# Performance work log

Measured on AMD Instinct MI355X. Metric: run time of the kernel, lower is better.

The kernel has to match this reference:

```python
import jax, jax.numpy as jnp
import numpy as np

C = 512      # channels
COND = 256   # cond_dim
H = 8        # n_heads
D = C // H   # head_dim
EPS = 1e-5


def setup_inputs() -> dict:
    key = jax.random.key(0)
    ks = jax.random.split(key, 16)
    s = 0.02
    inp = {
        "x": jax.random.normal(ks[0], (8, C, 1024), jnp.float32),
        "cond": jax.random.normal(ks[1], (8, COND), jnp.float32),
        "ln_g": jnp.ones((C,), jnp.float32),
        "ln_b": jnp.zeros((C,), jnp.float32),
        "Wq": jax.random.normal(ks[2], (C, C), jnp.float32) * s,
        "bq": jnp.zeros((C,), jnp.float32),
        "Wk": jax.random.normal(ks[3], (C, COND), jnp.float32) * s,
        "bk": jnp.zeros((C,), jnp.float32),
        "Wv": jax.random.normal(ks[4], (C, COND), jnp.float32) * s,
        "bv": jnp.zeros((C,), jnp.float32),
        "in_proj_w": jax.random.normal(ks[5], (3 * C, C), jnp.float32) * s,
        "in_proj_b": jnp.zeros((3 * C,), jnp.float32),
        "out_w": jax.random.normal(ks[6], (C, C), jnp.float32) * s,
        "out_b": jnp.zeros((C,), jnp.float32),
        "proj_w": jax.random.normal(ks[7], (C, C), jnp.float32) * s,
        "proj_b": jnp.zeros((C,), jnp.float32),
    }
    return inp


def _forward(x, cond, ln_g, ln_b, Wq, bq, Wk, bk, Wv, bv,
             in_proj_w, in_proj_b, out_w, out_b, proj_w, proj_b):
    B, _, T = x.shape
    x_seq = jnp.transpose(x, (0, 2, 1))                      # [B,T,C]
    mu = jnp.mean(x_seq, axis=-1, keepdims=True)
    var = jnp.mean((x_seq - mu) ** 2, axis=-1, keepdims=True)
    x_norm = (x_seq - mu) / jnp.sqrt(var + EPS) * ln_g + ln_b

    q = x_norm @ Wq.T + bq                                   # [B,T,C]
    k = cond @ Wk.T + bk                                     # [B,C]
    v = cond @ Wv.T + bv                                     # [B,C]

    # nn.MultiheadAttention internal input projections
    wq2, wk2, wv2 = in_proj_w[:C], in_proj_w[C:2 * C], in_proj_w[2 * C:]
    bq2, bk2, bv2 = in_proj_b[:C], in_proj_b[C:2 * C], in_proj_b[2 * C:]
    q2 = q @ wq2.T + bq2                                     # [B,T,C]
    k2 = k @ wk2.T + bk2                                     # [B,C]
    v2 = v @ wv2.T + bv2                                     # [B,C]

    qh = q2.reshape(B, T, H, D)                              # [B,T,H,D]
    kh = k2.reshape(B, H, D)
    vh = v2.reshape(B, H, D)

    # k/v are expanded to length T in the original module -> [B,T,C]
    k_exp = jnp.broadcast_to(kh[:, None, :, :], (B, T, H, D))
    v_exp = jnp.broadcast_to(vh[:, None, :, :], (B, T, H, D))

    scale = 1.0 / jnp.sqrt(jnp.float32(D))
    scores = jnp.einsum('bthd,bshd->bhts', qh * scale, k_exp)  # [B,H,T,T]
    attn = jax.nn.softmax(scores, axis=-1)
    outh = jnp.einsum('bhts,bshd->bthd', attn, v_exp)          # [B,T,H,D]
    out = outh.reshape(B, T, C) @ out_w.T + out_b              # MHA out_proj

    out = out @ proj_w.T + proj_b                              # self.proj
    out = jnp.transpose(out, (0, 2, 1))                        # [B,C,T]
    return x + out


def reference(x, cond, ln_g, ln_b, Wq, bq, Wk, bk, Wv, bv,
              in_proj_w, in_proj_b, out_w, out_b, proj_w, proj_b):
    return _forward(x, cond, ln_g, ln_b, Wq, bq, Wk, bk, Wv, bv,
                    in_proj_w, in_proj_b, out_w, out_b, proj_w, proj_b)
```

## Files before the change

### kernel.cpp

```cpp
#include <hip/hip_runtime.h>

#define CC   512
#define CONDK 256
#define BB   8
#define TT   1024

template<int K>
__global__ void gemv_kernel(const float* __restrict__ W, const float* __restrict__ bias,
                            const float* __restrict__ in, float* __restrict__ out) {
    const int wave = threadIdx.x >> 6;
    const int lane = threadIdx.x & 63;
    const int c = blockIdx.x * 4 + wave;
    const int b = blockIdx.y;
    const float* wrow = W + (size_t)c * K;
    const float* inb  = in + (size_t)b * K;
    float acc = 0.f;
#pragma unroll
    for (int j = lane; j < K; j += 64)
        acc += wrow[j] * inb[j];
#pragma unroll
    for (int off = 32; off >= 1; off >>= 1)
        acc += __shfl_down(acc, off, 64);
    if (lane == 0)
        out[b * CC + c] = acc + bias[c];
}

__global__ void add_bcast_kernel(const float* __restrict__ x, const float* __restrict__ w,
                                 float* __restrict__ out) {
    const int total4 = BB * CC * TT / 4;
    const float4* x4 = (const float4*)x;
    float4* o4 = (float4*)out;
    for (int i = blockIdx.x * blockDim.x + threadIdx.x; i < total4;
         i += gridDim.x * blockDim.x) {
        const int bc = i >> 8;
        const float a = w[bc];
        float4 v = x4[i];
        v.x += a; v.y += a; v.z += a; v.w += a;
        o4[i] = v;
    }
}

extern "C" void kernel_launch(void* const* d_in, const int* in_sizes, int n_in,
                              void* d_out, int out_size, void* d_ws, size_t ws_size,
                              hipStream_t stream) {
    const float* x         = (const float*)d_in[0];
    const float* cond      = (const float*)d_in[1];
    const float* Wv        = (const float*)d_in[8];
    const float* bv        = (const float*)d_in[9];
    const float* in_proj_w = (const float*)d_in[10];
    const float* in_proj_b = (const float*)d_in[11];
    const float* out_w     = (const float*)d_in[12];
    const float* out_b     = (const float*)d_in[13];
    const float* proj_w    = (const float*)d_in[14];
    const float* proj_b    = (const float*)d_in[15];
    float* out = (float*)d_out;

    float* v1 = (float*)d_ws;
    float* v2 = v1 + BB * CC;
    float* u  = v2 + BB * CC;
    float* w  = u  + BB * CC;

    dim3 blk(256);
    dim3 g1(CC / 4, BB);
    gemv_kernel<CONDK><<<g1, blk, 0, stream>>>(Wv, bv, cond, v1);
    gemv_kernel<CC><<<g1, blk, 0, stream>>>(in_proj_w + 2 * CC * CC, in_proj_b + 2 * CC, v1, v2);
    gemv_kernel<CC><<<g1, blk, 0, stream>>>(out_w, out_b, v2, u);
    gemv_kernel<CC><<<g1, blk, 0, stream>>>(proj_w, proj_b, u, w);

    add_bcast_kernel<<<1024, 256, 0, stream>>>(x, w, out);
}
```

Measured before the change: 22.48 us.

## Precombine proj and out weights, fuse final GEMV with broadcast add

Computes L1 = proj_w·out_w as a 512x512 matrix product and t = proj_w·out_b + proj_b in the first kernel, alongside the cond→v1 GEMV, so the two trailing GEMVs become one. The last GEMV is fused into the broadcast-add kernel, with each wave computing one (b,c) scalar and then streaming its row of x. This cuts five launches to three and removes a dependent GEMV stage. The cost is a full 512^3 weight product recomputed on every call and a different floating-point summation order.

New measurement: 31.14 us. 38.5% more time.

```diff
diff --git a/kernel.cpp b/kernel.cpp
--- a/kernel.cpp
+++ b/kernel.cpp
@@ -1,42 +1,108 @@
 #include <hip/hip_runtime.h>
 
-#define CC   512
-#define CONDK 256
-#define BB   8
-#define TT   1024
+#define CC 512
+#define CK 256
+#define BB 8
+#define TT 1024
 
-template<int K>
-__global__ void gemv_kernel(const float* __restrict__ W, const float* __restrict__ bias,
-                            const float* __restrict__ in, float* __restrict__ out) {
-    const int wave = threadIdx.x >> 6;
-    const int lane = threadIdx.x & 63;
-    const int c = blockIdx.x * 4 + wave;
-    const int b = blockIdx.y;
-    const float* wrow = W + (size_t)c * K;
-    const float* inb  = in + (size_t)b * K;
+__device__ __forceinline__ float wave_allreduce(float v) {
+#pragma unroll
+    for (int m = 1; m < 64; m <<= 1)
+        v += __shfl_xor(v, m, 64);
+    return v;
+}
+
+__global__ void k1_kernel(const float* __restrict__ P, const float* __restrict__ O,
+                          const float* __restrict__ Wv, const float* __restrict__ bv,
+                          const float* __restrict__ ob, const float* __restrict__ pb,
+                          const float* __restrict__ cond,
+                          float* __restrict__ L1, float* __restrict__ t,
+                          float* __restrict__ v1) {
+    const int blk = blockIdx.x;
+    const int tid = threadIdx.x;
+    const int wave = tid >> 6, lane = tid & 63;
+
+    if (blk < 256) {
+        __shared__ float As[32][33];
+        __shared__ float Bs[32][33];
+        const int ti = (blk >> 4) * 32, tj = (blk & 15) * 32;
+        const int lrow = tid >> 3, lc4 = (tid & 7) * 4;
+        const int ty = tid >> 4, tx = tid & 15;
+        float a00 = 0.f, a01 = 0.f, a10 = 0.f, a11 = 0.f;
+        for (int k = 0; k < 512; k += 32) {
+            __syncthreads();
+            *(float4*)&As[lrow][lc4] = *(const float4*)&P[(ti + lrow) * 512 + k + lc4];
+            *(float4*)&Bs[lrow][lc4] = *(const float4*)&O[(k + lrow) * 512 + tj + lc4];
+            __syncthreads();
+#pragma unroll
+            for (int kk = 0; kk < 32; ++kk) {
+                const float x0 = As[2 * ty][kk], x1 = As[2 * ty + 1][kk];
+                const float y0 = Bs[kk][2 * tx], y1 = Bs[kk][2 * tx + 1];
+                a00 += x0 * y0; a01 += x0 * y1; a10 += x1 * y0; a11 += x1 * y1;
+            }
+        }
+        float* d = L1 + (ti + 2 * ty) * 512 + tj + 2 * tx;
+        d[0] = a00; d[1] = a01; d[512] = a10; d[513] = a11;
+    } else if (blk < 384) {
+        const int gw = (blk - 256) * 4 + wave;
+#pragma unroll
+        for (int r = 0; r < 8; ++r) {
+            const int o = gw * 8 + r;
+            const int b = o >> 9, c = o & 511;
+            float acc = 0.f;
+#pragma unroll
+            for (int j = 0; j < CK; j += 64)
+                acc += Wv[c * CK + j + lane] * cond[b * CK + j + lane];
+            acc = wave_allreduce(acc);
+            if (lane == 0) v1[o] = acc + bv[c];
+        }
+    } else {
+        const int c = (blk - 384) * 4 + wave;
+        float acc = 0.f;
+#pragma unroll
+        for (int k = 0; k < CC; k += 64)
+            acc += P[c * CC + k + lane] * ob[k + lane];
+        acc = wave_allreduce(acc);
+        if (lane == 0) t[c] = acc + pb[c];
+    }
+}
+
+__global__ void k2_kernel(const float* __restrict__ wv2, const float* __restrict__ b2,
+                          const float* __restrict__ v1, float* __restrict__ v2) {
+    const int wave = threadIdx.x >> 6, lane = threadIdx.x & 63;
+    const int gw = blockIdx.x * 4 + wave;
+#pragma unroll
+    for (int r = 0; r < 4; ++r) {
+        const int o = gw * 4 + r;
+        const int b = o >> 9, c = o & 511;
+        float acc = 0.f;
+#pragma unroll
+        for (int j = 0; j < CC; j += 64)
+            acc += wv2[c * CC + j + lane] * v1[b * CC + j + lane];
+        acc = wave_allreduce(acc);
+        if (lane == 0) v2[o] = acc + b2[c];
+    }
+}
+
+__global__ void k3_kernel(const float* __restrict__ L1, const float* __restrict__ t,
+                          const float* __restrict__ v2, const float* __restrict__ x,
+                          float* __restrict__ out) {
+    const int wave = threadIdx.x >> 6, lane = threadIdx.x & 63;
+    const int o = blockIdx.x * 4 + wave;
+    const int b = o >> 9, c = o & 511;
     float acc = 0.f;
 #pragma unroll
-    for (int j = lane; j < K; j += 64)
-        acc += wrow[j] * inb[j];
+    for (int j = 0; j < CC; j += 64)
+        acc += L1[c * CC + j + lane] * v2[b * CC + j + lane];
+    const float w = wave_allreduce(acc) + t[c];
+
+    const float4* x4 = (const float4*)x + (size_t)o * (TT / 4);
+    float4* o4 = (float4*)out + (size_t)o * (TT / 4);
 #pragma unroll
-    for (int off = 32; off >= 1; off >>= 1)
-        acc += __shfl_down(acc, off, 64);
-    if (lane == 0)
-        out[b * CC + c] = acc + bias[c];
-}
-
-__global__ void add_bcast_kernel(const float* __restrict__ x, const float* __restrict__ w,
-                                 float* __restrict__ out) {
-    const int total4 = BB * CC * TT / 4;
-    const float4* x4 = (const float4*)x;
-    float4* o4 = (float4*)out;
-    for (int i = blockIdx.x * blockDim.x + threadIdx.x; i < total4;
-         i += gridDim.x * blockDim.x) {
-        const int bc = i >> 8;
-        const float a = w[bc];
-        float4 v = x4[i];
-        v.x += a; v.y += a; v.z += a; v.w += a;
-        o4[i] = v;
+    for (int i = 0; i < TT / 4; i += 64) {
+        float4 v = x4[i + lane];
+        v.x += w; v.y += w; v.z += w; v.w += w;
+        o4[i + lane] = v;
     }
 }
 
@@ -55,17 +121,14 @@
     const float* proj_b    = (const float*)d_in[15];
     float* out = (float*)d_out;
 
-    float* v1 = (float*)d_ws;
+    float* L1 = (float*)d_ws;
+    float* t  = L1 + CC * CC;
+    float* v1 = t + CC;
     float* v2 = v1 + BB * CC;
-    float* u  = v2 + BB * CC;
-    float* w  = u  + BB * CC;
 
-    dim3 blk(256);
-    dim3 g1(CC / 4, BB);
-    gemv_kernel<CONDK><<<g1, blk, 0, stream>>>(Wv, bv, cond, v1);
-    gemv_kernel<CC><<<g1, blk, 0, stream>>>(in_proj_w + 2 * CC * CC, in_proj_b + 2 * CC, v1, v2);
-    gemv_kernel<CC><<<g1, blk, 0, stream>>>(out_w, out_b, v2, u);
-    gemv_kernel<CC><<<g1, blk, 0, stream>>>(proj_w, proj_b, u, w);
-
-    add_bcast_kernel<<<1024, 256, 0, stream>>>(x, w, out);
+    k1_kernel<<<512, 256, 0, stream>>>(proj_w, out_w, Wv, bv, out_b, proj_b,
+                                       cond, L1, t, v1);
+    k2_kernel<<<256, 256, 0, stream>>>(in_proj_w + 2 * CC * CC, in_proj_b + 2 * CC,
+                                       v1, v2);
+    k3_kernel<<<1024, 256, 0, stream>>>(L1, t, v2, x, out);
 }
```
